# Optimization experiments

Measured on AMD Instinct MI355X. Metric: run time of the kernel, lower is better.

The kernel has to match this reference:

```python
import jax, jax.numpy as jnp
import numpy as np

LAYER_SPECS = [(2, 4, 1), (2, 4, 1), (1, 4, 1), (1, 4, 1)]
SKIPS = [(k - s) * d for (s, k, d) in LAYER_SPECS]  # (ksz-stride)*dilation
C = 80  # encoder channels


def _conv1d(x, w, b, stride, dilation):
    # x: (N, Cin, L), w: (Cout, Cin, K)
    out = jax.lax.conv_general_dilated(
        x, w, window_strides=(stride,), padding='VALID',
        rhs_dilation=(dilation,), dimension_numbers=('NCH', 'OIH', 'NCH'))
    return out + b[None, :, None]


def _encoder(x, w_wide, b_wide, w_1x1, b_1x1, w_f0, b_f0, w_f1, b_f1):
    # x: (N, T, 80) -> (N, T', 80)
    x = jnp.transpose(x, (0, 2, 1))  # (N, 80, T)
    for i, ((stride, ksz, dil), skip) in enumerate(zip(LAYER_SPECS, SKIPS)):
        x1 = _conv1d(x, w_wide[i], b_wide[i], stride, dil)  # (N, 2C, L')
        a, g = jnp.split(x1, 2, axis=1)
        x2 = jnp.tanh(a) * jax.nn.sigmoid(g)                # gated activation
        x3 = _conv1d(x2, w_1x1[i], b_1x1[i], 1, 1)          # (N, C, L')
        if i == 0:
            x = x3
        else:
            T3 = x3.shape[2]
            # residual: strided slice of previous x, take last of each stride group
            res = x[:, :, skip:skip + T3 * stride].reshape(x.shape[0], C, T3, stride)[:, :, :, -1]
            x = x3 + res
    x = _conv1d(jax.nn.relu(_conv1d(x, w_f0, b_f0, 1, 1)), w_f1, b_f1, 1, 1)
    return jnp.transpose(x, (0, 2, 1))  # (N, T', 80)


def setup_inputs() -> dict:
    key = jax.random.key(0)
    ks = jax.random.split(key, 10)
    N, Ts, Tq = 16, 8192, 2048
    return {
        'search': jax.random.normal(ks[0], (N, Ts, 80), dtype=jnp.float32),
        'query': jax.random.normal(ks[1], (N, Tq, 80), dtype=jnp.float32),
        'w_wide': jax.random.normal(ks[2], (4, 160, 80, 4), dtype=jnp.float32) * 0.02,
        'b_wide': jnp.zeros((4, 160), dtype=jnp.float32),
        'w_1x1': jax.random.normal(ks[3], (4, 80, 80, 1), dtype=jnp.float32) * 0.05,
        'b_1x1': jnp.zeros((4, 80), dtype=jnp.float32),
        'w_f0': jax.random.normal(ks[4], (80, 80, 1), dtype=jnp.float32) * 0.05,
        'b_f0': jnp.zeros((80,), dtype=jnp.float32),
        'w_f1': jax.random.normal(ks[5], (80, 80, 1), dtype=jnp.float32) * 0.05,
        'b_f1': jax.random.normal(ks[6], (80,), dtype=jnp.float32) * 0.05,
        'embedding': jax.random.normal(ks[7], (1, 512, 80), dtype=jnp.float32) * 0.001,
        'w_lin': jax.random.normal(ks[8], (2, 80), dtype=jnp.float32) * 0.05,
        'b_lin': jnp.zeros((2,), dtype=jnp.float32),
    }


def reference(search, query, w_wide, b_wide, w_1x1, b_1x1,
              w_f0, b_f0, w_f1, b_f1, embedding, w_lin, b_lin):
    enc_s = _encoder(search, w_wide, b_wide, w_1x1, b_1x1, w_f0, b_f0, w_f1, b_f1)
    enc_q = _encoder(query, w_wide, b_wide, w_1x1, b_1x1, w_f0, b_f0, w_f1, b_f1)

    # ---- VectorQuant (no normalize): nearest-codeword lookup + straight-through ----
    x = enc_s[:, :, None, :]                  # (N, T, 1, V)
    N, T, nc, V = x.shape
    n_classes = embedding.shape[1]
    x1 = x.reshape(N * T, nc, V)              # (NT, 1, V)
    # squared-distance via expansion: argmin identical to argmin of L2 norm
    x2 = jnp.sum(x1 * x1, axis=-1, keepdims=True)          # (NT, 1, 1)
    e2 = jnp.sum(embedding * embedding, axis=-1)[None]     # (1, 1, K)
    xe = jnp.einsum('ncv,ckv->nck', x1, embedding)         # (NT, 1, K)
    idx = jnp.argmin(x2 - 2.0 * xe + e2, axis=2)           # (NT, 1)
    offset = jnp.arange(nc) * n_classes
    flat = embedding.reshape(-1, V)
    output = flat[(idx + offset[None, :]).reshape(-1)].reshape(x.shape)
    out0 = jax.lax.stop_gradient(output - x) + x           # straight-through
    discrete = out0[:, :, 0, :]               # (N, Ts', V)

    # ---- align query to search length, classify, max-pool over time ----
    sf = discrete.shape[1] // enc_q.shape[1]
    q = jnp.tile(enc_q, (1, sf, 1))
    pad = discrete.shape[1] - q.shape[1]
    q = jnp.pad(q, ((0, 0), (0, pad), (0, 0)))
    pred = jnp.tanh((q + discrete) @ w_lin.T + b_lin)      # (N, Ts', 2)
    return jnp.max(pred, axis=1)                           # (N, 2)
```

## Files before the change

### kernel.cpp

```cpp
#include <hip/hip_runtime.h>
#include <math.h>


#define NBATCH 16

typedef __attribute__((ext_vector_type(8))) short s16x8;
typedef __attribute__((ext_vector_type(4))) float f32x4;

__device__ __forceinline__ float fast_sigmoid(float x){ return 1.0f/(1.0f+__expf(-x)); }
__device__ __forceinline__ float fast_tanh(float x){ return 2.0f/(1.0f+__expf(-2.0f*x))-1.0f; }
__device__ __forceinline__ unsigned short f2bf(float f){
    unsigned int u = __float_as_uint(f);
    return (unsigned short)((u + 0x7FFFu + ((u >> 16) & 1u)) >> 16);
}
__device__ __forceinline__ unsigned int pk2bf(float lo, float hi){
    unsigned int r;
    asm("v_cvt_pk_bf16_f32 %0, %1, %2" : "=v"(r) : "v"(lo), "v"(hi));
    return r;
}

__global__ __launch_bounds__(256) void pack_all(
    const float* __restrict__ w_wide, const float* __restrict__ w_1x1,
    const float* __restrict__ wf0,    const float* __restrict__ wf1,
    const float* __restrict__ emb,
    unsigned short* __restrict__ WW, unsigned short* __restrict__ W1,
    unsigned short* __restrict__ F0, unsigned short* __restrict__ F1,
    unsigned short* __restrict__ EM, float* __restrict__ e2o)
{
    int i = blockIdx.x * 256 + threadIdx.x;
    if (i < 204800) {
        int l = i / 51200, r = i % 51200, oc = r / 320, k = r % 320;
        int j = k / 80, ic = k % 80;
        WW[i] = f2bf(w_wide[l * 51200 + oc * 320 + ic * 4 + j]);
    } else if (i < 235520) {
        int idx = i - 204800, l = idx / 7680, r = idx % 7680, oc = r / 96, k = r % 96;
        W1[idx] = (k < 80) ? f2bf(w_1x1[l * 6400 + oc * 80 + k]) : (unsigned short)0;
    } else if (i < 243200) {
        int idx = i - 235520, oc = idx / 96, k = idx % 96;
        F0[idx] = (k < 80) ? f2bf(wf0[oc * 80 + k]) : (unsigned short)0;
    } else if (i < 250880) {
        int idx = i - 243200, oc = idx / 96, k = idx % 96;
        F1[idx] = (k < 80) ? f2bf(wf1[oc * 80 + k]) : (unsigned short)0;
    } else if (i < 291840) {
        EM[i - 250880] = f2bf(emb[i - 250880]);
    } else if (i < 292352) {
        int e = i - 291840;
        float s = 0.f;
        for (int k = 0; k < 80; ++k) { float v = emb[e * 80 + k]; s = fmaf(v, v, s); }
        e2o[e] = s;
    }
}

template<int S, bool HAS_RES, bool FINAL>
__global__ __launch_bounds__(320, 2) void enc_layer(
    const float* __restrict__ xS, const float* __restrict__ xQ,
    const unsigned short* __restrict__ ww,  const float* __restrict__ wb,
    const unsigned short* __restrict__ w1p, const float* __restrict__ b1,
    const unsigned short* __restrict__ f0p, const float* __restrict__ bf0,
    const unsigned short* __restrict__ f1p, const float* __restrict__ bf1,
    float* __restrict__ outS, float* __restrict__ outQ,
    int TinS, int ToutS, int TinQ, int ToutQ, int nbS)
{
    constexpr int TILE = 64;
    constexpr int MT   = 4;
    constexpr int P    = 63 * S + 4;
    constexpr int HALF = (S == 2) ? 65 : 67;
    constexpr int NPARY = (S == 2) ? 2 : 1;
    constexpr int XSTR = 104;
    constexpr int NEL  = P * 20;
    constexpr int NST  = (NEL + 319) / 320;

    __shared__ __attribute__((aligned(16))) unsigned short xs[NPARY * HALF * XSTR];
    __shared__ __attribute__((aligned(16))) unsigned short gsA[TILE * 104];
    __shared__ __attribute__((aligned(16))) unsigned short gsB[FINAL ? TILE * 104 : 8];

    const int tid  = threadIdx.x;
    const int wave = tid >> 6;
    const int lane = tid & 63;
    const int m    = lane & 15;
    const int quad = lane >> 4;
    const int n_   = blockIdx.y;

    const float* x; float* out; int T_in, T_out, bx;
    if ((int)blockIdx.x < nbS) { x = xS; out = outS; T_in = TinS; T_out = ToutS; bx = blockIdx.x; }
    else                       { x = xQ; out = outQ; T_in = TinQ; T_out = ToutQ; bx = blockIdx.x - nbS; }
    const int t0 = bx * TILE;
    const long base_in = (long)n_ * T_in * 80;

    float4 vst[NST]; int odx[NST]; bool okw[NST];
#pragma unroll
    for (int it = 0; it < NST; ++it) {
        int u = tid + it * 320;
        okw[it] = (u < NEL);
        if (u >= NEL) u = NEL - 1;
        int pos = u / 20, c4 = u % 20;
        int tp = t0 * S + pos; if (tp > T_in - 1) tp = T_in - 1;
        vst[it] = *(const float4*)(x + base_in + (long)tp * 80 + c4 * 4);
        int row = (S == 2) ? (pos >> 1) : pos;
        int par = (S == 2) ? (pos & 1) : 0;
        odx[it] = (par * HALF + row) * XSTR + c4 * 4;
    }

    const int quad8 = quad * 8;
    const unsigned short* wa_base = ww + (long)(wave * 16 + m) * 320 + quad8;
    const unsigned short* wg_base = ww + (long)((wave + 5) * 16 + m) * 320 + quad8;
    s16x8 wA[10], wG[10];
#pragma unroll
    for (int kk = 0; kk < 10; ++kk) {
        wA[kk] = *(const s16x8*)(wa_base + kk * 32);
        wG[kk] = *(const s16x8*)(wg_base + kk * 32);
    }
    const unsigned short* wb1 = w1p + (long)(wave * 16 + m) * 96 + quad8;
    s16x8 w1b0 = *(const s16x8*)(wb1);
    s16x8 w1b1 = *(const s16x8*)(wb1 + 32);
    s16x8 w1b2 = *(const s16x8*)(wb1 + 64);
    const float ba_b = wb[wave * 16 + m];
    const float bg_b = wb[80 + wave * 16 + m];
    const int c = wave * 16 + m;
    const float b1c = b1[c];

#pragma unroll
    for (int it = 0; it < NST; ++it) {
        if (okw[it]) {
            float4 v = vst[it];
            *(uint2*)&xs[odx[it]] = make_uint2(pk2bf(v.x, v.y), pk2bf(v.z, v.w));
        }
    }

    f32x4 acc_a[MT], acc_g[MT];
#pragma unroll
    for (int mt = 0; mt < MT; ++mt) {
        acc_a[mt] = (f32x4){0.f, 0.f, 0.f, 0.f};
        acc_g[mt] = (f32x4){0.f, 0.f, 0.f, 0.f};
    }

    __syncthreads();

#pragma unroll
    for (int kk = 0; kk < 10; ++kk) {
        const int kq = kk * 32 + quad8;
        const int j  = (kq >= 240) ? 3 : ((kq >= 160) ? 2 : ((kq >= 80) ? 1 : 0));
        const int ic0 = kq - j * 80;
        int xb;
        if (S == 2) xb = ((j & 1) * HALF + (j >> 1)) * XSTR + ic0;
        else        xb = j * XSTR + ic0;
        s16x8 a[MT];
#pragma unroll
        for (int mt = 0; mt < MT; ++mt)
            a[mt] = *(const s16x8*)&xs[xb + (mt * 16 + m) * XSTR];
#pragma unroll
        for (int mt = 0; mt < MT; ++mt) {
            acc_a[mt] = __builtin_amdgcn_mfma_f32_16x16x32_bf16(a[mt], wA[kk], acc_a[mt], 0, 0, 0);
            acc_g[mt] = __builtin_amdgcn_mfma_f32_16x16x32_bf16(a[mt], wG[kk], acc_g[mt], 0, 0, 0);
        }
    }

#pragma unroll
    for (int mt = 0; mt < MT; ++mt)
#pragma unroll
        for (int r = 0; r < 4; ++r) {
            float av = acc_a[mt][r] + ba_b;
            float gv = acc_g[mt][r] + bg_b;
            gsA[(mt * 16 + quad * 4 + r) * 104 + c] =
                f2bf(fast_tanh(av) * fast_sigmoid(gv));
        }
    const uint4 z4 = make_uint4(0u, 0u, 0u, 0u);
    {
        constexpr int NPAD = FINAL ? 256 : 128;
        for (int u = tid; u < NPAD; u += 320) {
            unsigned short* g = (u < 128) ? gsA : gsB;
            int v = u & 127;
            *(uint4*)&g[(v >> 1) * 104 + 80 + (v & 1) * 8] = z4;
        }
    }
    __syncthreads();

    auto mm96 = [&](s16x8 b0, s16x8 b1f, s16x8 b2, const unsigned short* g, f32x4 (&o)[MT]) {
#pragma unroll
        for (int mt = 0; mt < MT; ++mt) o[mt] = (f32x4){0.f, 0.f, 0.f, 0.f};
#pragma unroll
        for (int kb = 0; kb < 3; ++kb) {
            s16x8 b = (kb == 0) ? b0 : ((kb == 1) ? b1f : b2);
#pragma unroll
            for (int mt = 0; mt < MT; ++mt) {
                s16x8 ag = *(const s16x8*)&g[(mt * 16 + m) * 104 + kb * 32 + quad8];
                o[mt] = __builtin_amdgcn_mfma_f32_16x16x32_bf16(ag, b, o[mt], 0, 0, 0);
            }
        }
    };

    f32x4 a1[MT];
    mm96(w1b0, w1b1, w1b2, gsA, a1);

    const long base_out = (long)n_ * T_out * 80;
    if (!FINAL) {
#pragma unroll
        for (int mt = 0; mt < MT; ++mt)
#pragma unroll
            for (int r = 0; r < 4; ++r) {
                int tg = t0 + mt * 16 + quad * 4 + r;
                if (tg < T_out) {
                    float v = a1[mt][r] + b1c;
                    if (HAS_RES)
                        v += x[base_in + (long)(3 + (long)tg * S) * 80 + c];
                    out[base_out + (long)tg * 80 + c] = v;
                }
            }
    } else {
        float x3[MT][4];
#pragma unroll
        for (int mt = 0; mt < MT; ++mt)
#pragma unroll
            for (int r = 0; r < 4; ++r) {
                int tg = t0 + mt * 16 + quad * 4 + r;
                int tc = (tg < T_out) ? tg : (T_out - 1);
                float v = a1[mt][r] + b1c;
                if (HAS_RES)
                    v += x[base_in + (long)(3 + (long)tc * S) * 80 + c];
                x3[mt][r] = v;
            }
        const unsigned short* wf0b = f0p + (long)c * 96 + quad8;
        s16x8 f0b0 = *(const s16x8*)(wf0b);
        s16x8 f0b1 = *(const s16x8*)(wf0b + 32);
        s16x8 f0b2 = *(const s16x8*)(wf0b + 64);
        const float bf0c = bf0[c];
#pragma unroll
        for (int mt = 0; mt < MT; ++mt)
#pragma unroll
            for (int r = 0; r < 4; ++r)
                gsB[(mt * 16 + quad * 4 + r) * 104 + c] = f2bf(x3[mt][r]);
        __syncthreads();
        f32x4 a2[MT];
        mm96(f0b0, f0b1, f0b2, gsB, a2);
        const unsigned short* wf1b = f1p + (long)c * 96 + quad8;
        s16x8 f1b0 = *(const s16x8*)(wf1b);
        s16x8 f1b1 = *(const s16x8*)(wf1b + 32);
        s16x8 f1b2 = *(const s16x8*)(wf1b + 64);
        const float bf1c = bf1[c];
#pragma unroll
        for (int mt = 0; mt < MT; ++mt)
#pragma unroll
            for (int r = 0; r < 4; ++r)
                gsA[(mt * 16 + quad * 4 + r) * 104 + c] =
                    f2bf(fmaxf(a2[mt][r] + bf0c, 0.f));
        __syncthreads();
        f32x4 a3[MT];
        mm96(f1b0, f1b1, f1b2, gsA, a3);
#pragma unroll
        for (int mt = 0; mt < MT; ++mt)
#pragma unroll
            for (int r = 0; r < 4; ++r) {
                int tg = t0 + mt * 16 + quad * 4 + r;
                if (tg < T_out)
                    out[base_out + (long)tg * 80 + c] = a3[mt][r] + bf1c;
            }
    }
}

__global__ __launch_bounds__(256, 2) void vq_mfma(
    const float* __restrict__ enc_s, const float* __restrict__ enc_q,
    const unsigned short* __restrict__ embp, const float* __restrict__ emb,
    const float* __restrict__ e2v,
    const float* __restrict__ w_lin, const float* __restrict__ b_lin,
    float* __restrict__ pred)
{
    __shared__ unsigned short xs[64 * 104];
    __shared__ unsigned short es[128 * 104];
    const uint4 z4 = make_uint4(0u, 0u, 0u, 0u);

    const int tid  = threadIdx.x;
    const int wave = tid >> 6;
    const int lane = tid & 63;
    const int m    = lane & 15;
    const int quad = lane >> 4;
    const int n    = blockIdx.y;
    const int t0   = blockIdx.x * 64;

    for (int u = tid; u < 64 * 20; u += 256) {
        int row = u / 20, c4 = u % 20;
        int t = t0 + row; if (t > 2039) t = 2039;
        float4 v = *(const float4*)(enc_s + ((long)n * 2040 + t) * 80 + c4 * 4);
        unsigned int s0 = (unsigned int)f2bf(v.x) | ((unsigned int)f2bf(v.y) << 16);
        unsigned int s1 = (unsigned int)f2bf(v.z) | ((unsigned int)f2bf(v.w) << 16);
        *(uint2*)&xs[row * 104 + c4 * 4] = make_uint2(s0, s1);
    }
    for (int u = tid; u < 128; u += 256)
        *(uint4*)&xs[(u >> 1) * 104 + 80 + (u & 1) * 8] = z4;
    __syncthreads();

    s16x8 af[3];
#pragma unroll
    for (int kb = 0; kb < 3; ++kb)
        af[kb] = *(const s16x8*)&xs[(wave * 16 + m) * 104 + kb * 32 + quad * 8];

    float best[4]; int bi[4];
#pragma unroll
    for (int r = 0; r < 4; ++r) { best[r] = 1e30f; bi[r] = 0; }

    for (int ch = 0; ch < 4; ++ch) {
        const int c0 = ch * 128;
        __syncthreads();
        for (int u = tid; u < 128 * 12; u += 256) {
            int el = u / 12, seg = u % 12;
            uint4 v = z4;
            if (seg < 10) v = *(const uint4*)(embp + (long)(c0 + el) * 80 + seg * 8);
            *(uint4*)&es[el * 104 + seg * 8] = v;
        }
        __syncthreads();

        f32x4 acc[8];
#pragma unroll
        for (int nt = 0; nt < 8; ++nt) acc[nt] = (f32x4){0.f, 0.f, 0.f, 0.f};
#pragma unroll
        for (int kb = 0; kb < 3; ++kb) {
            const int k0 = kb * 32 + quad * 8;
#pragma unroll
            for (int nt = 0; nt < 8; ++nt) {
                s16x8 b = *(const s16x8*)&es[(nt * 16 + m) * 104 + k0];
                acc[nt] = __builtin_amdgcn_mfma_f32_16x16x32_bf16(af[kb], b, acc[nt], 0, 0, 0);
            }
        }
#pragma unroll
        for (int nt = 0; nt < 8; ++nt) {
            const int e = c0 + nt * 16 + m;
            const float e2x = e2v[e];
#pragma unroll
            for (int r = 0; r < 4; ++r) {
                float s = fmaf(-2.0f, acc[nt][r], e2x);
                if (s < best[r]) { best[r] = s; bi[r] = e; }
            }
        }
    }

    __syncthreads();
    float* rb = (float*)es;
    int*   ri = (int*)es + 1088;
#pragma unroll
    for (int r = 0; r < 4; ++r) {
        int tl = wave * 16 + quad * 4 + r;
        rb[tl * 17 + m] = best[r];
        ri[tl * 17 + m] = bi[r];
    }
    __syncthreads();

    if (tid < 64) {
        const int t = t0 + tid;
        float b = rb[tid * 17]; int ix = ri[tid * 17];
#pragma unroll
        for (int j = 1; j < 16; ++j) {
            float v = rb[tid * 17 + j]; int iv = ri[tid * 17 + j];
            if (v < b || (v == b && iv < ix)) { b = v; ix = iv; }
        }
        if (t < 2040) {
            const float4* ev = (const float4*)(emb + (long)ix * 80);
            const bool hasq = (t < 2016);
            const float4* qv = hasq
                ? (const float4*)(enc_q + ((long)n * 504 + (t % 504)) * 80) : nullptr;
            float p0 = b_lin[0], p1 = b_lin[1];
#pragma unroll
            for (int i = 0; i < 20; ++i) {
                float4 e4 = ev[i];
                float4 q4 = hasq ? qv[i] : make_float4(0.f, 0.f, 0.f, 0.f);
                float4 w0 = *(const float4*)(w_lin + 4 * i);
                float4 w1 = *(const float4*)(w_lin + 80 + 4 * i);
                float sx = e4.x + q4.x, sy = e4.y + q4.y;
                float sz = e4.z + q4.z, sw = e4.w + q4.w;
                p0 = fmaf(sx, w0.x, p0); p1 = fmaf(sx, w1.x, p1);
                p0 = fmaf(sy, w0.y, p0); p1 = fmaf(sy, w1.y, p1);
                p0 = fmaf(sz, w0.z, p0); p1 = fmaf(sz, w1.z, p1);
                p0 = fmaf(sw, w0.w, p0); p1 = fmaf(sw, w1.w, p1);
            }
            long o = ((long)n * 2040 + t) * 2;
            pred[o]     = fast_tanh(p0);
            pred[o + 1] = fast_tanh(p1);
        }
    }
}

__global__ __launch_bounds__(256) void max_red(const float* __restrict__ pred,
                                               float* __restrict__ out)
{
    __shared__ float s0[256], s1[256];
    const int n = blockIdx.x, tid = threadIdx.x;
    float m0 = -1e30f, m1 = -1e30f;
    for (int t = tid; t < 2040; t += 256) {
        long o = ((long)n * 2040 + t) * 2;
        m0 = fmaxf(m0, pred[o]);
        m1 = fmaxf(m1, pred[o + 1]);
    }
    s0[tid] = m0; s1[tid] = m1;
    __syncthreads();
    for (int st = 128; st > 0; st >>= 1) {
        if (tid < st) {
            s0[tid] = fmaxf(s0[tid], s0[tid + st]);
            s1[tid] = fmaxf(s1[tid], s1[tid + st]);
        }
        __syncthreads();
    }
    if (tid == 0) { out[n * 2] = s0[0]; out[n * 2 + 1] = s1[0]; }
}

extern "C" void kernel_launch(void* const* d_in, const int* in_sizes, int n_in,
                              void* d_out, int out_size, void* d_ws, size_t ws_size,
                              hipStream_t stream)
{
    const float* search = (const float*)d_in[0];
    const float* query  = (const float*)d_in[1];
    const float* w_wide = (const float*)d_in[2];
    const float* b_wide = (const float*)d_in[3];
    const float* w_1x1  = (const float*)d_in[4];
    const float* b_1x1  = (const float*)d_in[5];
    const float* w_f0   = (const float*)d_in[6];
    const float* b_f0   = (const float*)d_in[7];
    const float* w_f1   = (const float*)d_in[8];
    const float* b_f1   = (const float*)d_in[9];
    const float* emb    = (const float*)d_in[10];
    const float* w_lin  = (const float*)d_in[11];
    const float* b_lin  = (const float*)d_in[12];
    float* out = (float*)d_out;
    float* ws  = (float*)d_ws;

    float* A  = ws;
    float* B  = A  + 5241600;
    float* C  = B  + 2618880;
    float* QA = C  + 2618880;
    float* QB = QA + 1309440;
    float* QC = QB + 652800;
    unsigned short* WWp = (unsigned short*)(QC + 652800);
    unsigned short* W1p = WWp + 204800;
    unsigned short* F0p = W1p + 30720;
    unsigned short* F1p = F0p + 7680;
    unsigned short* EMp = F1p + 7680;
    float* e2b = (float*)(EMp + 40960);

    const dim3 blk(320);
    auto nb = [](int T) { return (T + 63) / 64; };

    pack_all<<<dim3(1142), dim3(256), 0, stream>>>(w_wide, w_1x1, w_f0, w_f1, emb,
                                                   WWp, W1p, F0p, F1p, EMp, e2b);

    enc_layer<2, false, false><<<dim3(nb(4095) + nb(1023), NBATCH), blk, 0, stream>>>(
        search, query, WWp, b_wide, W1p, b_1x1, nullptr, nullptr, nullptr, nullptr,
        A, QA, 8192, 4095, 2048, 1023, nb(4095));
    enc_layer<2, true, false><<<dim3(nb(2046) + nb(510), NBATCH), blk, 0, stream>>>(
        A, QA, WWp + 51200, b_wide + 160, W1p + 7680, b_1x1 + 80,
        nullptr, nullptr, nullptr, nullptr,
        B, QB, 4095, 2046, 1023, 510, nb(2046));
    enc_layer<1, true, false><<<dim3(nb(2043) + nb(507), NBATCH), blk, 0, stream>>>(
        B, QB, WWp + 102400, b_wide + 320, W1p + 15360, b_1x1 + 160,
        nullptr, nullptr, nullptr, nullptr,
        C, QC, 2046, 2043, 510, 507, nb(2043));
    enc_layer<1, true, true><<<dim3(nb(2040) + nb(504), NBATCH), blk, 0, stream>>>(
        C, QC, WWp + 153600, b_wide + 480, W1p + 23040, b_1x1 + 240,
        F0p, b_f0, F1p, b_f1,
        B, QB, 2043, 2040, 507, 504, nb(2040));

    vq_mfma<<<dim3(32, NBATCH), dim3(256), 0, stream>>>(B, QB, EMp, emb, e2b,
                                                        w_lin, b_lin, C);
    max_red<<<dim3(NBATCH), dim3(256), 0, stream>>>(C, out);
}
```

Before: 267.4 us.

## Cut encoder register pressure, stream weights, tighten LDS stride, parallelize argmin tail

```diff
diff --git a/kernel.cpp b/kernel.cpp
--- a/kernel.cpp
+++ b/kernel.cpp
@@ -17,6 +17,9 @@
     unsigned int r;
     asm("v_cvt_pk_bf16_f32 %0, %1, %2" : "=v"(r) : "v"(lo), "v"(hi));
     return r;
+}
+__device__ __forceinline__ unsigned short cvt1bf(float v){
+    return (unsigned short)pk2bf(v, v);
 }
 
 __global__ __launch_bounds__(256) void pack_all(
@@ -52,7 +55,7 @@
 }
 
 template<int S, bool HAS_RES, bool FINAL>
-__global__ __launch_bounds__(320, 2) void enc_layer(
+__global__ __launch_bounds__(320, 3) void enc_layer(
     const float* __restrict__ xS, const float* __restrict__ xQ,
     const unsigned short* __restrict__ ww,  const float* __restrict__ wb,
     const unsigned short* __restrict__ w1p, const float* __restrict__ b1,
@@ -61,30 +64,30 @@
     float* __restrict__ outS, float* __restrict__ outQ,
     int TinS, int ToutS, int TinQ, int ToutQ, int nbS)
 {
-    constexpr int TILE = 64;
     constexpr int MT   = 4;
     constexpr int P    = 63 * S + 4;
     constexpr int HALF = (S == 2) ? 65 : 67;
-    constexpr int NPARY = (S == 2) ? 2 : 1;
-    constexpr int XSTR = 104;
+    constexpr int NPARY= (S == 2) ? 2 : 1;
     constexpr int NEL  = P * 20;
     constexpr int NST  = (NEL + 319) / 320;
 
-    __shared__ __attribute__((aligned(16))) unsigned short xs[NPARY * HALF * XSTR];
-    __shared__ __attribute__((aligned(16))) unsigned short gsA[TILE * 104];
-    __shared__ __attribute__((aligned(16))) unsigned short gsB[FINAL ? TILE * 104 : 8];
+    __shared__ __attribute__((aligned(16))) unsigned short xs[NPARY * HALF * 88];
+    __shared__ __attribute__((aligned(16))) unsigned short gsA[64 * 104];
+    __shared__ __attribute__((aligned(16))) unsigned short gsB[FINAL ? 64 * 104 : 8];
 
     const int tid  = threadIdx.x;
     const int wave = tid >> 6;
     const int lane = tid & 63;
     const int m    = lane & 15;
     const int quad = lane >> 4;
+    const int quad8 = quad * 8;
+    const int c    = wave * 16 + m;
     const int n_   = blockIdx.y;
 
     const float* x; float* out; int T_in, T_out, bx;
     if ((int)blockIdx.x < nbS) { x = xS; out = outS; T_in = TinS; T_out = ToutS; bx = blockIdx.x; }
     else                       { x = xQ; out = outQ; T_in = TinQ; T_out = ToutQ; bx = blockIdx.x - nbS; }
-    const int t0 = bx * TILE;
+    const int t0 = bx * 64;
     const long base_in = (long)n_ * T_in * 80;
 
     float4 vst[NST]; int odx[NST]; bool okw[NST];
@@ -98,26 +101,31 @@
         vst[it] = *(const float4*)(x + base_in + (long)tp * 80 + c4 * 4);
         int row = (S == 2) ? (pos >> 1) : pos;
         int par = (S == 2) ? (pos & 1) : 0;
-        odx[it] = (par * HALF + row) * XSTR + c4 * 4;
-    }
-
-    const int quad8 = quad * 8;
-    const unsigned short* wa_base = ww + (long)(wave * 16 + m) * 320 + quad8;
-    const unsigned short* wg_base = ww + (long)((wave + 5) * 16 + m) * 320 + quad8;
-    s16x8 wA[10], wG[10];
-#pragma unroll
-    for (int kk = 0; kk < 10; ++kk) {
-        wA[kk] = *(const s16x8*)(wa_base + kk * 32);
-        wG[kk] = *(const s16x8*)(wg_base + kk * 32);
-    }
-    const unsigned short* wb1 = w1p + (long)(wave * 16 + m) * 96 + quad8;
+        odx[it] = (par * HALF + row) * 88 + c4 * 4;
+    }
+
+    const unsigned short* wa_base = ww + (long)c * 320 + quad8;
+    const unsigned short* wg_base = ww + (long)(80 + c) * 320 + quad8;
+    s16x8 baP[3], bgP[3];
+    baP[0] = *(const s16x8*)(wa_base);       bgP[0] = *(const s16x8*)(wg_base);
+    baP[1] = *(const s16x8*)(wa_base + 32);  bgP[1] = *(const s16x8*)(wg_base + 32);
+
+    const unsigned short* wb1 = w1p + (long)c * 96 + quad8;
     s16x8 w1b0 = *(const s16x8*)(wb1);
     s16x8 w1b1 = *(const s16x8*)(wb1 + 32);
     s16x8 w1b2 = *(const s16x8*)(wb1 + 64);
-    const float ba_b = wb[wave * 16 + m];
-    const float bg_b = wb[80 + wave * 16 + m];
-    const int c = wave * 16 + m;
-    const float b1c = b1[c];
+
+    float resv[16];
+    if (HAS_RES) {
+#pragma unroll
+        for (int mt = 0; mt < MT; ++mt)
+#pragma unroll
+            for (int r = 0; r < 4; ++r) {
+                int tg = t0 + mt * 16 + quad * 4 + r;
+                if (tg > T_out - 1) tg = T_out - 1;
+                resv[mt * 4 + r] = x[base_in + (long)(3 + (long)tg * S) * 80 + c];
+            }
+    }
 
 #pragma unroll
     for (int it = 0; it < NST; ++it) {
@@ -138,23 +146,30 @@
 
 #pragma unroll
     for (int kk = 0; kk < 10; ++kk) {
+        if (kk + 2 < 10) {
+            baP[(kk + 2) % 3] = *(const s16x8*)(wa_base + (kk + 2) * 32);
+            bgP[(kk + 2) % 3] = *(const s16x8*)(wg_base + (kk + 2) * 32);
+        }
         const int kq = kk * 32 + quad8;
         const int j  = (kq >= 240) ? 3 : ((kq >= 160) ? 2 : ((kq >= 80) ? 1 : 0));
         const int ic0 = kq - j * 80;
         int xb;
-        if (S == 2) xb = ((j & 1) * HALF + (j >> 1)) * XSTR + ic0;
-        else        xb = j * XSTR + ic0;
+        if (S == 2) xb = ((j & 1) * HALF + (j >> 1)) * 88 + ic0;
+        else        xb = j * 88 + ic0;
         s16x8 a[MT];
 #pragma unroll
         for (int mt = 0; mt < MT; ++mt)
-            a[mt] = *(const s16x8*)&xs[xb + (mt * 16 + m) * XSTR];
+            a[mt] = *(const s16x8*)&xs[xb + (mt * 16 + m) * 88];
+        s16x8 ba = baP[kk % 3], bg = bgP[kk % 3];
 #pragma unroll
         for (int mt = 0; mt < MT; ++mt) {
-            acc_a[mt] = __builtin_amdgcn_mfma_f32_16x16x32_bf16(a[mt], wA[kk], acc_a[mt], 0, 0, 0);
-            acc_g[mt] = __builtin_amdgcn_mfma_f32_16x16x32_bf16(a[mt], wG[kk], acc_g[mt], 0, 0, 0);
-        }
-    }
-
+            acc_a[mt] = __builtin_amdgcn_mfma_f32_16x16x32_bf16(a[mt], ba, acc_a[mt], 0, 0, 0);
+            acc_g[mt] = __builtin_amdgcn_mfma_f32_16x16x32_bf16(a[mt], bg, acc_g[mt], 0, 0, 0);
+        }
+    }
+
+    const float ba_b = wb[c];
+    const float bg_b = wb[80 + c];
 #pragma unroll
     for (int mt = 0; mt < MT; ++mt)
 #pragma unroll
@@ -162,7 +177,7 @@
             float av = acc_a[mt][r] + ba_b;
             float gv = acc_g[mt][r] + bg_b;
             gsA[(mt * 16 + quad * 4 + r) * 104 + c] =
-                f2bf(fast_tanh(av) * fast_sigmoid(gv));
+                cvt1bf(fast_tanh(av) * fast_sigmoid(gv));
         }
     const uint4 z4 = make_uint4(0u, 0u, 0u, 0u);
     {
@@ -193,6 +208,7 @@
     mm96(w1b0, w1b1, w1b2, gsA, a1);
 
     const long base_out = (long)n_ * T_out * 80;
+    const float b1c = b1[c];
     if (!FINAL) {
 #pragma unroll
         for (int mt = 0; mt < MT; ++mt)
@@ -201,8 +217,7 @@
                 int tg = t0 + mt * 16 + quad * 4 + r;
                 if (tg < T_out) {
                     float v = a1[mt][r] + b1c;
-                    if (HAS_RES)
-                        v += x[base_in + (long)(3 + (long)tg * S) * 80 + c];
+                    if (HAS_RES) v += resv[mt * 4 + r];
                     out[base_out + (long)tg * 80 + c] = v;
                 }
             }
@@ -212,11 +227,8 @@
         for (int mt = 0; mt < MT; ++mt)
 #pragma unroll
             for (int r = 0; r < 4; ++r) {
-                int tg = t0 + mt * 16 + quad * 4 + r;
-                int tc = (tg < T_out) ? tg : (T_out - 1);
                 float v = a1[mt][r] + b1c;
-                if (HAS_RES)
-                    v += x[base_in + (long)(3 + (long)tc * S) * 80 + c];
+                if (HAS_RES) v += resv[mt * 4 + r];
                 x3[mt][r] = v;
             }
         const unsigned short* wf0b = f0p + (long)c * 96 + quad8;
@@ -228,7 +240,7 @@
         for (int mt = 0; mt < MT; ++mt)
 #pragma unroll
             for (int r = 0; r < 4; ++r)
-                gsB[(mt * 16 + quad * 4 + r) * 104 + c] = f2bf(x3[mt][r]);
+                gsB[(mt * 16 + quad * 4 + r) * 104 + c] = cvt1bf(x3[mt][r]);
         __syncthreads();
         f32x4 a2[MT];
         mm96(f0b0, f0b1, f0b2, gsB, a2);
@@ -242,7 +254,7 @@
 #pragma unroll
             for (int r = 0; r < 4; ++r)
                 gsA[(mt * 16 + quad * 4 + r) * 104 + c] =
-                    f2bf(fmaxf(a2[mt][r] + bf0c, 0.f));
+                    cvt1bf(fmaxf(a2[mt][r] + bf0c, 0.f));
         __syncthreads();
         f32x4 a3[MT];
         mm96(f1b0, f1b1, f1b2, gsA, a3);
@@ -280,9 +292,7 @@
         int row = u / 20, c4 = u % 20;
         int t = t0 + row; if (t > 2039) t = 2039;
         float4 v = *(const float4*)(enc_s + ((long)n * 2040 + t) * 80 + c4 * 4);
-        unsigned int s0 = (unsigned int)f2bf(v.x) | ((unsigned int)f2bf(v.y) << 16);
-        unsigned int s1 = (unsigned int)f2bf(v.z) | ((unsigned int)f2bf(v.w) << 16);
-        *(uint2*)&xs[row * 104 + c4 * 4] = make_uint2(s0, s1);
+        *(uint2*)&xs[row * 104 + c4 * 4] = make_uint2(pk2bf(v.x, v.y), pk2bf(v.z, v.w));
     }
     for (int u = tid; u < 128; u += 256)
         *(uint4*)&xs[(u >> 1) * 104 + 80 + (u & 1) * 8] = z4;
@@ -333,8 +343,10 @@
     }
 
     __syncthreads();
-    float* rb = (float*)es;
-    int*   ri = (int*)es + 1088;
+    float* rb  = (float*)es;
+    int*   ri  = (int*)es + 1088;
+    float* rb2 = (float*)es + 2176;
+    int*   ri2 = (int*)es + 2432;
 #pragma unroll
     for (int r = 0; r < 4; ++r) {
         int tl = wave * 16 + quad * 4 + r;
@@ -343,36 +355,46 @@
     }
     __syncthreads();
 
-    if (tid < 64) {
-        const int t = t0 + tid;
-        float b = rb[tid * 17]; int ix = ri[tid * 17];
-#pragma unroll
-        for (int j = 1; j < 16; ++j) {
-            float v = rb[tid * 17 + j]; int iv = ri[tid * 17 + j];
+    {
+        const int t = tid >> 2, g = tid & 3;
+        const int o = t * 17 + g * 4;
+        float b = rb[o]; int ix = ri[o];
+#pragma unroll
+        for (int j = 1; j < 4; ++j) {
+            float v = rb[o + j]; int iv = ri[o + j];
             if (v < b || (v == b && iv < ix)) { b = v; ix = iv; }
         }
+        rb2[t * 4 + g] = b; ri2[t * 4 + g] = ix;
+    }
+    __syncthreads();
+
+    if (tid < 128) {
+        const int trow = tid >> 1, h = tid & 1;
+        float b = rb2[trow * 4]; int ix = ri2[trow * 4];
+#pragma unroll
+        for (int j = 1; j < 4; ++j) {
+            float v = rb2[trow * 4 + j]; int iv = ri2[trow * 4 + j];
+            if (v < b || (v == b && iv < ix)) { b = v; ix = iv; }
+        }
+        const int t = t0 + trow;
         if (t < 2040) {
             const float4* ev = (const float4*)(emb + (long)ix * 80);
             const bool hasq = (t < 2016);
             const float4* qv = hasq
                 ? (const float4*)(enc_q + ((long)n * 504 + (t % 504)) * 80) : nullptr;
-            float p0 = b_lin[0], p1 = b_lin[1];
+            const float4* wl = (const float4*)(w_lin + h * 80);
+            float p = b_lin[h];
 #pragma unroll
             for (int i = 0; i < 20; ++i) {
                 float4 e4 = ev[i];
                 float4 q4 = hasq ? qv[i] : make_float4(0.f, 0.f, 0.f, 0.f);
-                float4 w0 = *(const float4*)(w_lin + 4 * i);
-                float4 w1 = *(const float4*)(w_lin + 80 + 4 * i);
-                float sx = e4.x + q4.x, sy = e4.y + q4.y;
-                float sz = e4.z + q4.z, sw = e4.w + q4.w;
-                p0 = fmaf(sx, w0.x, p0); p1 = fmaf(sx, w1.x, p1);
-                p0 = fmaf(sy, w0.y, p0); p1 = fmaf(sy, w1.y, p1);
-                p0 = fmaf(sz, w0.z, p0); p1 = fmaf(sz, w1.z, p1);
-                p0 = fmaf(sw, w0.w, p0); p1 = fmaf(sw, w1.w, p1);
-            }
-            long o = ((long)n * 2040 + t) * 2;
-            pred[o]     = fast_tanh(p0);
-            pred[o + 1] = fast_tanh(p1);
+                float4 w4 = wl[i];
+                p = fmaf(e4.x + q4.x, w4.x, p);
+                p = fmaf(e4.y + q4.y, w4.y, p);
+                p = fmaf(e4.z + q4.z, w4.z, p);
+                p = fmaf(e4.w + q4.w, w4.w, p);
+            }
+            pred[((long)n * 2040 + t) * 2 + h] = fast_tanh(p);
         }
     }
 }
```

Measured after the change: 254.3 us. 4.9% less time.
